# Performance work log

Measured on AMD Instinct MI355X. Metric: run time of the kernel, lower is better.

The kernel has to match this reference:

```python
import jax, jax.numpy as jnp
import numpy as np

D_IN = 1024
D_OUT = 1024
N_HEADS = 16
HEAD_DIM = D_OUT // N_HEADS


def setup_inputs() -> dict:
    key = jax.random.key(0)
    ks = jax.random.split(key, 6)
    s = 0.02
    x = jax.random.normal(ks[0], (2, 2048, D_IN), dtype=jnp.float32)
    Wq = jax.random.normal(ks[1], (D_IN, D_OUT), dtype=jnp.float32) * s
    Wk = jax.random.normal(ks[2], (D_IN, D_OUT), dtype=jnp.float32) * s
    Wv = jax.random.normal(ks[3], (D_IN, D_OUT), dtype=jnp.float32) * s
    Wo = jax.random.normal(ks[4], (D_OUT, D_OUT), dtype=jnp.float32) * s
    bo = jax.random.normal(ks[5], (D_OUT,), dtype=jnp.float32) * s
    return {"x": x, "Wq": Wq, "Wk": Wk, "Wv": Wv, "Wo": Wo, "bo": bo}


def reference(x, Wq, Wk, Wv, Wo, bo):
    B, S, _ = x.shape
    # project and split heads: (B, H, S, Dh)
    def split(t):
        return t.reshape(B, S, N_HEADS, HEAD_DIM).transpose(0, 2, 1, 3)
    q = split(x @ Wq)
    k = split(x @ Wk)
    v = split(x @ Wv)
    scores = jnp.einsum('bhqd,bhkd->bhqk', q, k)  # (B,H,S,S)
    causal = jnp.tril(jnp.ones((S, S), dtype=bool))
    scores = jnp.where(causal, scores, -jnp.inf)
    attn = jax.nn.softmax(scores / np.sqrt(HEAD_DIM).astype(np.float32), axis=-1)
    ctx = jnp.einsum('bhqk,bhkd->bhqd', attn, v)
    ctx = ctx.transpose(0, 2, 1, 3).reshape(B, S, D_OUT)
    return ctx @ Wo + bo
```

## Files before the change

kernel.cpp:

```cpp
#include <hip/hip_runtime.h>
#include <hip/hip_bf16.h>
#include <math.h>

typedef __attribute__((ext_vector_type(8))) short bf16x8;
typedef __attribute__((ext_vector_type(8))) unsigned short u16x8;
typedef __attribute__((ext_vector_type(4))) float f32x4;

__device__ __forceinline__ unsigned short f2bf(float f) {
  union { float f; unsigned u; } c; c.f = f;
  unsigned u = c.u;
  u += 0x7fffu + ((u >> 16) & 1u);
  return (unsigned short)(u >> 16);
}
__device__ __forceinline__ unsigned fb(float x) {
  union { float f; unsigned u; } c; c.f = x; return c.u;
}
__device__ __forceinline__ void async16(const unsigned short* g, unsigned short* l) {
  __builtin_amdgcn_global_load_lds(
      (const __attribute__((address_space(1))) unsigned int*)g,
      (__attribute__((address_space(3))) unsigned int*)l, 16, 0, 0);
}

__global__ __launch_bounds__(256) void cast_kernel(const float* __restrict__ in,
                                                   unsigned short* __restrict__ out,
                                                   int n4) {
  int i = blockIdx.x * 256 + threadIdx.x;
  if (i >= n4) return;
  float4 v = ((const float4*)in)[i];
  ushort4 o;
  o.x = f2bf(v.x); o.y = f2bf(v.y); o.z = f2bf(v.z); o.w = f2bf(v.w);
  ((ushort4*)out)[i] = o;
}

__global__ __launch_bounds__(256) void transpose_cast(
    const float* __restrict__ Wq, const float* __restrict__ Wk,
    const float* __restrict__ Wv, const float* __restrict__ Wo,
    unsigned short* __restrict__ Wqkvt, unsigned short* __restrict__ Wot) {
  __shared__ float t[32][33];
  int z = blockIdx.z;
  const float* src = (z == 0) ? Wq : (z == 1) ? Wk : (z == 2) ? Wv : Wo;
  unsigned short* dst = (z < 3) ? (Wqkvt + (size_t)z * 1024 * 1024) : Wot;
  int tx = threadIdx.x & 31, ty = threadIdx.x >> 5;
  int bx = blockIdx.x, by = blockIdx.y;
#pragma unroll
  for (int i = 0; i < 4; ++i)
    t[ty + i * 8][tx] = src[(size_t)(by * 32 + ty + i * 8) * 1024 + bx * 32 + tx];
  __syncthreads();
#pragma unroll
  for (int i = 0; i < 4; ++i)
    dst[(size_t)(bx * 32 + ty + i * 8) * 1024 + by * 32 + tx] = f2bf(t[tx][ty + i * 8]);
}

__global__ __launch_bounds__(256) void gemm_qkv(
    const unsigned short* __restrict__ A, const unsigned short* __restrict__ Bt,
    unsigned short* __restrict__ Qh, unsigned short* __restrict__ Kh,
    unsigned short* __restrict__ Vt, int K) {
  __shared__ unsigned short As[128][32];
  __shared__ unsigned short Bs[128][32];
  const int tid = threadIdx.x;
  const int wave = tid >> 6, lane = tid & 63;
  const int quad = lane >> 4, l16 = lane & 15;
  const int m0 = blockIdx.y * 128, n0 = blockIdx.x * 128;
  const int wm = (wave >> 1) * 64, wn = (wave & 1) * 64;
  const int srow = tid >> 2, sch = (tid & 3) * 8;
  f32x4 acc[4][4] = {};

  for (int k0 = 0; k0 < K; k0 += 32) {
    __syncthreads();
    async16(A  + (size_t)(m0 + srow) * K + k0 + sch, &As[srow][sch]);
    async16(Bt + (size_t)(n0 + srow) * K + k0 + sch, &Bs[srow][sch]);
    async16(A  + (size_t)(m0 + srow + 64) * K + k0 + sch, &As[srow + 64][sch]);
    async16(Bt + (size_t)(n0 + srow + 64) * K + k0 + sch, &Bs[srow + 64][sch]);
    __syncthreads();
    bf16x8 af[4], bfr[4];
#pragma unroll
    for (int i = 0; i < 4; ++i) {
      af[i]  = *(const bf16x8*)&As[wm + i * 16 + l16][quad * 8];
      bfr[i] = *(const bf16x8*)&Bs[wn + i * 16 + l16][quad * 8];
    }
#pragma unroll
    for (int mi = 0; mi < 4; ++mi)
#pragma unroll
      for (int ni = 0; ni < 4; ++ni)
        acc[mi][ni] = __builtin_amdgcn_mfma_f32_16x16x32_bf16(af[mi], bfr[ni], acc[mi][ni], 0, 0, 0);
  }

#pragma unroll
  for (int mi = 0; mi < 4; ++mi) {
#pragma unroll
    for (int ni = 0; ni < 4; ++ni) {
      const int col = n0 + wn + ni * 16 + l16;
      const int token0 = m0 + wm + mi * 16 + quad * 4;
      const int bb = token0 >> 11, s0 = token0 & 2047;
      if (col < 2048) {
        const int hh = (col & 1023) >> 6, d = col & 63;
        unsigned short* dst = (col < 1024) ? Qh : Kh;
        dst += ((size_t)(bb * 16 + hh) * 2048 + s0) * 64 + d;
#pragma unroll
        for (int r = 0; r < 4; ++r) dst[(size_t)r * 64] = f2bf(acc[mi][ni][r]);
      } else {
        const int vc = col - 2048, hh = vc >> 6, d = vc & 63;
        ushort4 us;
        us.x = f2bf(acc[mi][ni][0]); us.y = f2bf(acc[mi][ni][1]);
        us.z = f2bf(acc[mi][ni][2]); us.w = f2bf(acc[mi][ni][3]);
        *(ushort4*)&Vt[(((size_t)(bb * 16 + hh) * 64 + (s0 >> 5)) * 64 + d) * 32 + (s0 & 31)] = us;
      }
    }
  }
}

__global__ __launch_bounds__(256) void gemm_out(
    const unsigned short* __restrict__ A, const unsigned short* __restrict__ Bt,
    float* __restrict__ C, const float* __restrict__ bias, int N, int K) {
  __shared__ unsigned short As[128][32];
  __shared__ unsigned short Bs[64][32];
  const int tid = threadIdx.x;
  const int wave = tid >> 6, lane = tid & 63;
  const int quad = lane >> 4, l16 = lane & 15;
  const int m0 = blockIdx.y * 128, n0 = blockIdx.x * 64;
  const int wm = (wave >> 1) * 64, wn = (wave & 1) * 32;
  const int srow = tid >> 2, sch = (tid & 3) * 8;
  f32x4 acc[4][2] = {};

  for (int k0 = 0; k0 < K; k0 += 32) {
    __syncthreads();
    async16(A  + (size_t)(m0 + srow) * K + k0 + sch, &As[srow][sch]);
    async16(A  + (size_t)(m0 + srow + 64) * K + k0 + sch, &As[srow + 64][sch]);
    async16(Bt + (size_t)(n0 + srow) * K + k0 + sch, &Bs[srow][sch]);
    __syncthreads();
    bf16x8 af[4], bfr[2];
#pragma unroll
    for (int i = 0; i < 4; ++i)
      af[i] = *(const bf16x8*)&As[wm + i * 16 + l16][quad * 8];
#pragma unroll
    for (int i = 0; i < 2; ++i)
      bfr[i] = *(const bf16x8*)&Bs[wn + i * 16 + l16][quad * 8];
#pragma unroll
    for (int mi = 0; mi < 4; ++mi)
#pragma unroll
      for (int ni = 0; ni < 2; ++ni)
        acc[mi][ni] = __builtin_amdgcn_mfma_f32_16x16x32_bf16(af[mi], bfr[ni], acc[mi][ni], 0, 0, 0);
  }
#pragma unroll
  for (int mi = 0; mi < 4; ++mi)
#pragma unroll
    for (int ni = 0; ni < 2; ++ni) {
      const int col = n0 + wn + ni * 16 + l16;
      const float bv = bias[col];
      const int row0 = m0 + wm + mi * 16 + quad * 4;
#pragma unroll
      for (int r = 0; r < 4; ++r)
        C[(size_t)(row0 + r) * N + col] = acc[mi][ni][r] + bv;
    }
}

__global__ __launch_bounds__(128, 3) void attn_kernel(
    const unsigned short* __restrict__ Qh, const unsigned short* __restrict__ Kh,
    const unsigned short* __restrict__ Vt, unsigned short* __restrict__ ctx) {
  const int id = blockIdx.x;
  const int j = id >> 3;
  const int bh = (id & 7) | ((j & 3) << 3);
  const int s = 63 - (j >> 2);
  const int b = bh >> 4, h = bh & 15;
  const int wave = threadIdx.x >> 6, lane = threadIdx.x & 63;
  const int quad = lane >> 4, l16 = lane & 15;
  const int q0 = s * 32;
  const int T = (s + 2) >> 1;
  const int lo = wave ? (T >> 1) : 0;
  const int hi = wave ? T : (T >> 1);

  __shared__ __align__(16) char smem[10752];
  unsigned short (*Pt)[32][72] = (unsigned short (*)[32][72])smem;
  float (*Os)[2][64][4] = (float (*)[2][64][4])smem;
  float (*Ms)[64] = (float (*)[64])(smem + 10240);

  const unsigned short* Qp = Qh + (size_t)bh * 2048 * 64;
  const unsigned short* Kg = Kh + (size_t)bh * 2048 * 64;
  const unsigned short* Vg = Vt + (size_t)bh * 64 * 2048;

  bf16x8 qf[2][2];
#pragma unroll
  for (int qg = 0; qg < 2; ++qg)
#pragma unroll
    for (int kk = 0; kk < 2; ++kk)
      qf[qg][kk] = *(const bf16x8*)(Qp + (size_t)(q0 + qg * 16 + l16) * 64 + kk * 32 + quad * 8);

  bf16x8 ones;
#pragma unroll
  for (int jj = 0; jj < 8; ++jj) ones[jj] = (short)0x3F80;

  f32x4 o[5][2] = {};
  float m_[2] = {-INFINITY, -INFINITY};
  const float C = 0.18033688f;

  for (int jt = lo; jt < hi; ++jt) {
    const int k0 = jt * 64;
    f32x4 st[4][2] = {};
#pragma unroll
    for (int keyg = 0; keyg < 4; ++keyg) {
#pragma unroll
      for (int kk = 0; kk < 2; ++kk) {
        bf16x8 kf = *(const bf16x8*)(Kg + (size_t)(k0 + keyg * 16 + l16) * 64 + kk * 32 + quad * 8);
#pragma unroll
        for (int qg = 0; qg < 2; ++qg)
          st[keyg][qg] = __builtin_amdgcn_mfma_f32_16x16x32_bf16(kf, qf[qg][kk], st[keyg][qg], 0, 0, 0);
      }
    }
    bf16x8 vf[4][2];
#pragma unroll
    for (int dg = 0; dg < 4; ++dg)
#pragma unroll
      for (int half = 0; half < 2; ++half)
        vf[dg][half] = *(const bf16x8*)(Vg + (size_t)(2 * jt + half) * 2048 + (dg * 16 + l16) * 32 + quad * 8);
    if (jt == T - 1) {
#pragma unroll
      for (int keyg = 0; keyg < 4; ++keyg)
#pragma unroll
        for (int r = 0; r < 4; ++r) {
          const int key = k0 + keyg * 16 + quad * 4 + r;
#pragma unroll
          for (int qg = 0; qg < 2; ++qg)
            if (key > q0 + qg * 16 + l16) st[keyg][qg][r] = -INFINITY;
        }
    }
    float al[2];
#pragma unroll
    for (int qg = 0; qg < 2; ++qg) {
      float mx = fmaxf(fmaxf(st[0][qg][0], st[0][qg][1]), fmaxf(st[0][qg][2], st[0][qg][3]));
#pragma unroll
      for (int keyg = 1; keyg < 4; ++keyg)
        mx = fmaxf(mx, fmaxf(fmaxf(st[keyg][qg][0], st[keyg][qg][1]),
                             fmaxf(st[keyg][qg][2], st[keyg][qg][3])));
      mx = fmaxf(mx, __shfl_xor(mx, 16));
      mx = fmaxf(mx, __shfl_xor(mx, 32));
      const float mn = fmaxf(m_[qg], mx * C);
      al[qg] = exp2f(m_[qg] - mn);
      m_[qg] = mn;
#pragma unroll
      for (int keyg = 0; keyg < 4; ++keyg) {
        float p0 = exp2f(fmaf(st[keyg][qg][0], C, -mn));
        float p1 = exp2f(fmaf(st[keyg][qg][1], C, -mn));
        float p2 = exp2f(fmaf(st[keyg][qg][2], C, -mn));
        float p3 = exp2f(fmaf(st[keyg][qg][3], C, -mn));
        uint2 pk;
        pk.x = __builtin_amdgcn_perm(fb(p1), fb(p0), 0x07060302u);
        pk.y = __builtin_amdgcn_perm(fb(p3), fb(p2), 0x07060302u);
        *(uint2*)&Pt[wave][qg * 16 + l16][keyg * 16 + quad * 4] = pk;
      }
    }
    if (__any(fminf(al[0], al[1]) < 1.0f)) {
#pragma unroll
      for (int dg = 0; dg < 5; ++dg)
#pragma unroll
        for (int qg = 0; qg < 2; ++qg)
#pragma unroll
          for (int r = 0; r < 4; ++r) o[dg][qg][r] *= al[qg];
    }
    bf16x8 pb[2][2];
#pragma unroll
    for (int qg = 0; qg < 2; ++qg)
#pragma unroll
      for (int half = 0; half < 2; ++half)
        pb[qg][half] = *(const bf16x8*)&Pt[wave][qg * 16 + l16][half * 32 + quad * 8];
#pragma unroll
    for (int dg = 0; dg < 4; ++dg)
#pragma unroll
      for (int qg = 0; qg < 2; ++qg) {
        o[dg][qg] = __builtin_amdgcn_mfma_f32_16x16x32_bf16(vf[dg][0], pb[qg][0], o[dg][qg], 0, 0, 0);
        o[dg][qg] = __builtin_amdgcn_mfma_f32_16x16x32_bf16(vf[dg][1], pb[qg][1], o[dg][qg], 0, 0, 0);
      }
#pragma unroll
    for (int qg = 0; qg < 2; ++qg) {
      o[4][qg] = __builtin_amdgcn_mfma_f32_16x16x32_bf16(ones, pb[qg][0], o[4][qg], 0, 0, 0);
      o[4][qg] = __builtin_amdgcn_mfma_f32_16x16x32_bf16(ones, pb[qg][1], o[4][qg], 0, 0, 0);
    }
  }
  __syncthreads();
  if (wave == 1) {
#pragma unroll
    for (int qg = 0; qg < 2; ++qg) {
      Ms[qg][lane] = m_[qg];
#pragma unroll
      for (int dg = 0; dg < 5; ++dg)
        *(f32x4*)&Os[dg][qg][lane][0] = o[dg][qg];
    }
  }
  __syncthreads();
  if (wave == 0) {
#pragma unroll
    for (int qg = 0; qg < 2; ++qg) {
      const float m1 = Ms[qg][lane];
      const float mn = fmaxf(m_[qg], m1);
      const float a0 = exp2f(m_[qg] - mn), a1 = exp2f(m1 - mn);
#pragma unroll
      for (int dg = 0; dg < 5; ++dg) {
        f32x4 o1 = *(const f32x4*)&Os[dg][qg][lane][0];
#pragma unroll
        for (int r = 0; r < 4; ++r) o[dg][qg][r] = o[dg][qg][r] * a0 + o1[r] * a1;
      }
      const float inv = 1.f / o[4][qg][0];
      const size_t base = (size_t)(b * 2048 + q0 + qg * 16 + l16) * 1024 + h * 64;
#pragma unroll
      for (int dg = 0; dg < 4; ++dg) {
        ushort4 us;
        us.x = f2bf(o[dg][qg][0] * inv); us.y = f2bf(o[dg][qg][1] * inv);
        us.z = f2bf(o[dg][qg][2] * inv); us.w = f2bf(o[dg][qg][3] * inv);
        *(ushort4*)&ctx[base + dg * 16 + quad * 4] = us;
      }
    }
  }
}

extern "C" void kernel_launch(void* const* d_in, const int* in_sizes, int n_in,
                              void* d_out, int out_size, void* d_ws, size_t ws_size,
                              hipStream_t stream) {
  const float* x  = (const float*)d_in[0];
  const float* Wq = (const float*)d_in[1];
  const float* Wk = (const float*)d_in[2];
  const float* Wv = (const float*)d_in[3];
  const float* Wo = (const float*)d_in[4];
  const float* bo = (const float*)d_in[5];
  float* out = (float*)d_out;

  char* ws = (char*)d_ws;
  unsigned short* Xb    = (unsigned short*)(ws);
  unsigned short* Wqkvt = (unsigned short*)(ws + (size_t)8  * 1048576);
  unsigned short* Wot   = (unsigned short*)(ws + (size_t)14 * 1048576);
  unsigned short* Qhb   = (unsigned short*)(ws + (size_t)16 * 1048576);
  unsigned short* Khb   = (unsigned short*)(ws + (size_t)24 * 1048576);
  unsigned short* Vtb   = (unsigned short*)(ws + (size_t)32 * 1048576);
  unsigned short* CT    = (unsigned short*)(ws + (size_t)40 * 1048576);

  cast_kernel<<<4096, 256, 0, stream>>>(x, Xb, 1048576);
  transpose_cast<<<dim3(32, 32, 4), 256, 0, stream>>>(Wq, Wk, Wv, Wo, Wqkvt, Wot);
  gemm_qkv<<<dim3(24, 32), 256, 0, stream>>>(Xb, Wqkvt, Qhb, Khb, Vtb, 1024);
  attn_kernel<<<2048, 128, 0, stream>>>(Qhb, Khb, Vtb, CT);
  gemm_out<<<dim3(16, 32), 256, 0, stream>>>(CT, Wot, out, bo, 1024, 1024);
}
```

Baseline: 201.2 us.

## Vectorize Q/K epilogue stores via swapped MFMA operands; prefetch next K tile

In the QKV GEMM, Q/K tiles now swap the MFMA operand order so each lane holds four consecutive head-dim values, which allows packed 8-byte stores instead of strided 2-byte scalar stores. In the attention loop, K fragments for the next key tile are loaded into registers while the current tile's scores are computed, hiding global load latency. The cost is more register pressure from the extra K fragment buffer, which could reduce occupancy, plus a uniform branch inside the GEMM k-loop.

```diff
diff --git a/kernel.cpp b/kernel.cpp
--- a/kernel.cpp
+++ b/kernel.cpp
@@ -63,6 +63,7 @@
   const int m0 = blockIdx.y * 128, n0 = blockIdx.x * 128;
   const int wm = (wave >> 1) * 64, wn = (wave & 1) * 64;
   const int srow = tid >> 2, sch = (tid & 3) * 8;
+  const bool qk = (n0 < 2048);
   f32x4 acc[4][4] = {};
 
   for (int k0 = 0; k0 < K; k0 += 32) {
@@ -78,27 +79,46 @@
       af[i]  = *(const bf16x8*)&As[wm + i * 16 + l16][quad * 8];
       bfr[i] = *(const bf16x8*)&Bs[wn + i * 16 + l16][quad * 8];
     }
-#pragma unroll
-    for (int mi = 0; mi < 4; ++mi)
-#pragma unroll
-      for (int ni = 0; ni < 4; ++ni)
-        acc[mi][ni] = __builtin_amdgcn_mfma_f32_16x16x32_bf16(af[mi], bfr[ni], acc[mi][ni], 0, 0, 0);
-  }
-
-#pragma unroll
-  for (int mi = 0; mi < 4; ++mi) {
-#pragma unroll
-    for (int ni = 0; ni < 4; ++ni) {
-      const int col = n0 + wn + ni * 16 + l16;
-      const int token0 = m0 + wm + mi * 16 + quad * 4;
-      const int bb = token0 >> 11, s0 = token0 & 2047;
-      if (col < 2048) {
-        const int hh = (col & 1023) >> 6, d = col & 63;
-        unsigned short* dst = (col < 1024) ? Qh : Kh;
-        dst += ((size_t)(bb * 16 + hh) * 2048 + s0) * 64 + d;
-#pragma unroll
-        for (int r = 0; r < 4; ++r) dst[(size_t)r * 64] = f2bf(acc[mi][ni][r]);
-      } else {
+    if (qk) {
+#pragma unroll
+      for (int mi = 0; mi < 4; ++mi)
+#pragma unroll
+        for (int ni = 0; ni < 4; ++ni)
+          acc[mi][ni] = __builtin_amdgcn_mfma_f32_16x16x32_bf16(bfr[ni], af[mi], acc[mi][ni], 0, 0, 0);
+    } else {
+#pragma unroll
+      for (int mi = 0; mi < 4; ++mi)
+#pragma unroll
+        for (int ni = 0; ni < 4; ++ni)
+          acc[mi][ni] = __builtin_amdgcn_mfma_f32_16x16x32_bf16(af[mi], bfr[ni], acc[mi][ni], 0, 0, 0);
+    }
+  }
+
+  if (qk) {
+#pragma unroll
+    for (int mi = 0; mi < 4; ++mi) {
+      const int token = m0 + wm + mi * 16 + l16;
+      const int bb = token >> 11, s0 = token & 2047;
+#pragma unroll
+      for (int ni = 0; ni < 4; ++ni) {
+        const int c0 = n0 + wn + ni * 16 + quad * 4;
+        const int hh = (c0 & 1023) >> 6, d0 = c0 & 63;
+        unsigned short* dst = ((c0 < 1024) ? Qh : Kh)
+            + ((size_t)(bb * 16 + hh) * 2048 + s0) * 64 + d0;
+        ushort4 us;
+        us.x = f2bf(acc[mi][ni][0]); us.y = f2bf(acc[mi][ni][1]);
+        us.z = f2bf(acc[mi][ni][2]); us.w = f2bf(acc[mi][ni][3]);
+        *(ushort4*)dst = us;
+      }
+    }
+  } else {
+#pragma unroll
+    for (int mi = 0; mi < 4; ++mi) {
+#pragma unroll
+      for (int ni = 0; ni < 4; ++ni) {
+        const int col = n0 + wn + ni * 16 + l16;
+        const int token0 = m0 + wm + mi * 16 + quad * 4;
+        const int bb = token0 >> 11, s0 = token0 & 2047;
         const int vc = col - 2048, hh = vc >> 6, d = vc & 63;
         ushort4 us;
         us.x = f2bf(acc[mi][ni][0]); us.y = f2bf(acc[mi][ni][1]);
@@ -193,25 +213,36 @@
   float m_[2] = {-INFINITY, -INFINITY};
   const float C = 0.18033688f;
 
+  bf16x8 kfc[4][2];
+#pragma unroll
+  for (int keyg = 0; keyg < 4; ++keyg)
+#pragma unroll
+    for (int kk = 0; kk < 2; ++kk)
+      kfc[keyg][kk] = *(const bf16x8*)(Kg + (size_t)(lo * 64 + keyg * 16 + l16) * 64 + kk * 32 + quad * 8);
+
   for (int jt = lo; jt < hi; ++jt) {
     const int k0 = jt * 64;
-    f32x4 st[4][2] = {};
-#pragma unroll
-    for (int keyg = 0; keyg < 4; ++keyg) {
-#pragma unroll
-      for (int kk = 0; kk < 2; ++kk) {
-        bf16x8 kf = *(const bf16x8*)(Kg + (size_t)(k0 + keyg * 16 + l16) * 64 + kk * 32 + quad * 8);
-#pragma unroll
-        for (int qg = 0; qg < 2; ++qg)
-          st[keyg][qg] = __builtin_amdgcn_mfma_f32_16x16x32_bf16(kf, qf[qg][kk], st[keyg][qg], 0, 0, 0);
-      }
-    }
     bf16x8 vf[4][2];
 #pragma unroll
     for (int dg = 0; dg < 4; ++dg)
 #pragma unroll
       for (int half = 0; half < 2; ++half)
         vf[dg][half] = *(const bf16x8*)(Vg + (size_t)(2 * jt + half) * 2048 + (dg * 16 + l16) * 32 + quad * 8);
+    f32x4 st[4][2] = {};
+#pragma unroll
+    for (int keyg = 0; keyg < 4; ++keyg)
+#pragma unroll
+      for (int kk = 0; kk < 2; ++kk)
+#pragma unroll
+        for (int qg = 0; qg < 2; ++qg)
+          st[keyg][qg] = __builtin_amdgcn_mfma_f32_16x16x32_bf16(kfc[keyg][kk], qf[qg][kk], st[keyg][qg], 0, 0, 0);
+    if (jt + 1 < hi) {
+#pragma unroll
+      for (int keyg = 0; keyg < 4; ++keyg)
+#pragma unroll
+        for (int kk = 0; kk < 2; ++kk)
+          kfc[keyg][kk] = *(const bf16x8*)(Kg + (size_t)(k0 + 64 + keyg * 16 + l16) * 64 + kk * 32 + quad * 8);
+    }
     if (jt == T - 1) {
 #pragma unroll
       for (int keyg = 0; keyg < 4; ++keyg)
```

New measurement: 232.9 us. 15.7% more time.
